# Kernel optimization log

Hardware: AMD Instinct MI355X
Metric: run time of the kernel (lower is better)

The kernel has to match this reference:

```python
import jax, jax.numpy as jnp
import numpy as np

GAMES = 16384
BOARD = 64


def setup_inputs() -> dict:
    key = jax.random.key(0)
    k_act, k_noise = jax.random.split(key)
    c = BOARD // 2
    # Replicate TensorSnake.init(): snake body=1 at (c-1,c-1), head=2 at (c-1,c), one food cell=-1.
    state = np.zeros((GAMES, BOARD, BOARD), dtype=np.float32)
    state[:, c - 1, c - 1] = 1.0
    state[:, c - 1, c] = 2.0
    state[:, 0, 0] = -1.0  # food
    pos_prev = np.tile(np.array([[c - 1, c - 1]], dtype=np.int32), (GAMES, 1))
    pos_cur = pos_prev + np.array([0, 1], dtype=np.int32)
    action = jax.random.randint(k_act, (GAMES,), 0, 3, dtype=jnp.int32)
    noise = jax.random.uniform(k_noise, (GAMES, BOARD * BOARD), dtype=jnp.float32)
    return {
        "state": jnp.asarray(state),
        "pos_prev": jnp.asarray(pos_prev),
        "pos_cur": jnp.asarray(pos_cur),
        "action": action,
        "noise": noise,
    }


def reference(state, pos_prev, pos_cur, action, noise):
    G, B, _ = state.shape
    g = jnp.arange(G)
    # --- direction update per action (0=left, 1=straight, 2=right) ---
    d = pos_cur - pos_prev  # [G,2]
    d_left = jnp.stack([-d[:, 1], d[:, 0]], axis=1)   # flip then negate x
    d_right = jnp.stack([d[:, 1], -d[:, 0]], axis=1)  # flip then negate y
    left = (action == 0)[:, None]
    right = (action == 2)[:, None]
    d = jnp.where(left, d_left, jnp.where(right, d_right, d))
    pos_next = d + pos_cur
    # --- wall collision / clamp ---
    outside = jnp.any((pos_next < 0) | (pos_next >= B), axis=1)
    pos_next = jnp.clip(pos_next, 0, B - 1)
    cell = state[g, pos_next[:, 0], pos_next[:, 1]]
    dead = outside | (cell > 0)
    feeding = cell == -1
    # --- reset dead games ---
    state = jnp.where(dead[:, None, None], jnp.zeros((), state.dtype), state)
    c = B // 2
    p2 = jnp.array([c, c], dtype=pos_next.dtype)
    pos_cur = jnp.where(dead[:, None], jnp.array([c, c - 1], dtype=pos_cur.dtype), pos_cur)
    pos_next = jnp.where(dead[:, None], p2, pos_next)
    state = state.at[:, c, c - 2].set(jnp.where(dead, 1.0, state[:, c, c - 2]))
    state = state.at[:, c, c - 1].set(jnp.where(dead, 2.0, state[:, c, c - 1]))
    state = state.at[:, c, c].set(jnp.where(dead, 1.0, state[:, c, c]))
    # --- food spawn: uniform choice among empty cells via masked argmax on uniform noise ---
    spawn = dead | feeding
    empty = state.reshape(G, -1) == 0
    food = jnp.argmax(jnp.where(empty, noise, -jnp.inf), axis=1)
    fx = food // B
    fy = food % B
    state = state.at[g, fx, fy].set(jnp.where(spawn, -1.0, state[g, fx, fy]))
    # --- tail decay (skipped for feeding games) ---
    dec = (state > 0) & (~feeding)[:, None, None]
    state = state - dec.astype(state.dtype)
    # --- advance head ---
    head = state[g, pos_cur[:, 0], pos_cur[:, 1]]
    state = state.at[g, pos_next[:, 0], pos_next[:, 1]].set(head + 1.0)
    return state
```

## Files before the change

kernel.cpp:

```cpp
#include <hip/hip_runtime.h>
#include <math.h>

#define NGAMES 16384
#define BRD 64
#define CELLS 4096
#define THREADS 128
#define CHUNKS 8
#define NWAVES (THREADS / 64)

typedef float f4 __attribute__((ext_vector_type(4)));

__global__ __launch_bounds__(THREADS) void snake_step_kernel(
    const float* __restrict__ state,
    const int*   __restrict__ pos_prev,
    const int*   __restrict__ pos_cur,
    const int*   __restrict__ action,
    const float* __restrict__ noise,
    float*       __restrict__ out)
{
    const int g = blockIdx.x;
    const int t = threadIdx.x;
    const float* sg = state + (size_t)g * CELLS;
    float*       og = out   + (size_t)g * CELLS;

    __shared__ float wv[NWAVES];
    __shared__ int   wi[NWAVES];
    __shared__ int   food_s;

    const int pp0 = pos_prev[2 * g], pp1 = pos_prev[2 * g + 1];
    const int pc0 = pos_cur[2 * g],  pc1 = pos_cur[2 * g + 1];
    const int a = action[g];
    const int d0 = pc0 - pp0, d1 = pc1 - pp1;
    int nd0 = d0, nd1 = d1;
    if (a == 0)      { nd0 = -d1; nd1 =  d0; }
    else if (a == 2) { nd0 =  d1; nd1 = -d0; }
    int pn0 = pc0 + nd0, pn1 = pc1 + nd1;
    const bool outside = (pn0 < 0) | (pn0 >= BRD) | (pn1 < 0) | (pn1 >= BRD);
    pn0 = min(max(pn0, 0), BRD - 1);
    pn1 = min(max(pn1, 0), BRD - 1);
    const int posn_spec = pn0 * BRD + pn1;
    const int posc_live = pc0 * BRD + pc1;

    const float cellv = sg[posn_spec];
    const float curv  = sg[posc_live];

    f4 v[CHUNKS];
    const f4* sg4 = reinterpret_cast<const f4*>(sg);
    #pragma unroll
    for (int k = 0; k < CHUNKS; ++k)
        v[k] = sg4[t + k * THREADS];

    #pragma unroll
    for (int k = 0; k < CHUNKS; ++k) {
        #pragma unroll
        for (int j = 0; j < 4; ++j)
            v[k][j] = (v[k][j] > 0.0f) ? v[k][j] - 1.0f : v[k][j];
    }

    const int  headF   = posn_spec >> 2;
    const int  headK   = headF >> 7;
    const bool ownHead = (t == (headF & (THREADS - 1)));

    f4* og4 = reinterpret_cast<f4*>(og);
    #pragma unroll
    for (int k = 0; k < CHUNKS; ++k)
        if (!(ownHead && k == headK))
            __builtin_nontemporal_store(v[k], &og4[t + k * THREADS]);

    const bool dead    = outside | (cellv > 0.0f);
    const bool feeding = (cellv == -1.0f);
    const bool rare    = dead | feeding;

    if (!rare) {
        if (ownHead) {
            const float headv = (curv > 0.0f) ? curv - 1.0f : curv;
            const float hv = headv + 1.0f;
            const int j = posn_spec & 3;
            #pragma unroll
            for (int k = 0; k < CHUNKS; ++k)
                if (k == headK) {
                    f4 w = v[k];
                    w[j] = hv;
                    __builtin_nontemporal_store(w, &og4[t + k * THREADS]);
                }
        }
        return;
    }

    __syncthreads();

    float s[CHUNKS * 4];
    f4* s4 = reinterpret_cast<f4*>(s);
    #pragma unroll
    for (int k = 0; k < CHUNKS; ++k)
        s4[k] = sg4[t + k * THREADS];

    if (dead) {
        #pragma unroll
        for (int k = 0; k < CHUNKS; ++k) {
            #pragma unroll
            for (int j = 0; j < 4; ++j) {
                const int idx = (t + k * THREADS) * 4 + j;
                float x = 0.0f;
                if (idx == 2078) x = 1.0f;
                else if (idx == 2079) x = 2.0f;
                else if (idx == 2080) x = 1.0f;
                s[k * 4 + j] = x;
            }
        }
    }

    {
        float bv = -INFINITY;
        int   bi = 0x7FFFFFFF;
        const f4* ng4 = reinterpret_cast<const f4*>(noise + (size_t)g * CELLS);
        #pragma unroll
        for (int k = 0; k < CHUNKS; ++k) {
            const f4 nv = ng4[t + k * THREADS];
            #pragma unroll
            for (int j = 0; j < 4; ++j) {
                const int idx = (t + k * THREADS) * 4 + j;
                if (s[k * 4 + j] == 0.0f) {
                    const float n = nv[j];
                    if (n > bv || (n == bv && idx < bi)) { bv = n; bi = idx; }
                }
            }
        }
        #pragma unroll
        for (int off = 32; off > 0; off >>= 1) {
            const float ov = __shfl_xor(bv, off, 64);
            const int   oi = __shfl_xor(bi, off, 64);
            if (ov > bv || (ov == bv && oi < bi)) { bv = ov; bi = oi; }
        }
        const int wave = t >> 6;
        if ((t & 63) == 0) { wv[wave] = bv; wi[wave] = bi; }
        __syncthreads();
        if (t == 0) {
            float fv = wv[0]; int fi = wi[0];
            #pragma unroll
            for (int w = 1; w < NWAVES; ++w)
                if (wv[w] > fv || (wv[w] == fv && wi[w] < fi)) { fv = wv[w]; fi = wi[w]; }
            food_s = (fv == -INFINITY) ? 0 : fi;
        }
        __syncthreads();
    }
    const int food = food_s;

    #pragma unroll
    for (int k = 0; k < CHUNKS; ++k) {
        #pragma unroll
        for (int j = 0; j < 4; ++j) {
            const int idx = (t + k * THREADS) * 4 + j;
            if (idx == food) s[k * 4 + j] = -1.0f;
            if (!feeding && s[k * 4 + j] > 0.0f) s[k * 4 + j] -= 1.0f;
        }
    }

    const int posc = dead ? (32 * BRD + 31) : posc_live;
    const int posn = dead ? (32 * BRD + 32) : posn_spec;
    float headv = dead ? 2.0f : curv;
    if (food == posc) headv = -1.0f;
    if (!feeding && headv > 0.0f) headv -= 1.0f;
    const float hv = headv + 1.0f;

    const int posnF = posn >> 2, posnJ = posn & 3;
    #pragma unroll
    for (int k = 0; k < CHUNKS; ++k) {
        f4 w = s4[k];
        if ((t + k * THREADS) == posnF) w[posnJ] = hv;
        og4[t + k * THREADS] = w;
    }
}

extern "C" void kernel_launch(void* const* d_in, const int* in_sizes, int n_in,
                              void* d_out, int out_size, void* d_ws, size_t ws_size,
                              hipStream_t stream) {
    const float* state    = (const float*)d_in[0];
    const int*   pos_prev = (const int*)d_in[1];
    const int*   pos_cur  = (const int*)d_in[2];
    const int*   action   = (const int*)d_in[3];
    const float* noise    = (const float*)d_in[4];
    float*       out      = (float*)d_out;

    snake_step_kernel<<<NGAMES, THREADS, 0, stream>>>(
        state, pos_prev, pos_cur, action, noise, out);
}
```

Before: 69.14 us.

## Map one wavefront per game with four games per block

Each 64-lane wavefront now owns a whole game, holding 16 float4 chunks per lane, and a block of 256 threads processes four games. This removes the shared-memory cross-wave argmax reduction and all __syncthreads, so the food-spawn path resolves with wave shuffles alone. The state load is issued before the scalar position loads to start memory traffic earlier. Per-lane register pressure doubles (64 floats held), which may lower occupancy on the bandwidth-bound copy.

```diff
diff --git a/kernel.cpp b/kernel.cpp
--- a/kernel.cpp
+++ b/kernel.cpp
@@ -4,9 +4,9 @@
 #define NGAMES 16384
 #define BRD 64
 #define CELLS 4096
-#define THREADS 128
-#define CHUNKS 8
-#define NWAVES (THREADS / 64)
+#define THREADS 256
+#define GPB 4
+#define CHUNKS 16
 
 typedef float f4 __attribute__((ext_vector_type(4)));
 
@@ -18,14 +18,17 @@
     const float* __restrict__ noise,
     float*       __restrict__ out)
 {
-    const int g = blockIdx.x;
-    const int t = threadIdx.x;
+    const int g    = blockIdx.x * GPB + (threadIdx.x >> 6);
+    const int lane = threadIdx.x & 63;
     const float* sg = state + (size_t)g * CELLS;
     float*       og = out   + (size_t)g * CELLS;
+    const f4* sg4 = reinterpret_cast<const f4*>(sg);
+    f4*       og4 = reinterpret_cast<f4*>(og);
 
-    __shared__ float wv[NWAVES];
-    __shared__ int   wi[NWAVES];
-    __shared__ int   food_s;
+    f4 v[CHUNKS];
+    #pragma unroll
+    for (int k = 0; k < CHUNKS; ++k)
+        v[k] = sg4[lane + k * 64];
 
     const int pp0 = pos_prev[2 * g], pp1 = pos_prev[2 * g + 1];
     const int pc0 = pos_cur[2 * g],  pc1 = pos_cur[2 * g + 1];
@@ -44,12 +47,6 @@
     const float cellv = sg[posn_spec];
     const float curv  = sg[posc_live];
 
-    f4 v[CHUNKS];
-    const f4* sg4 = reinterpret_cast<const f4*>(sg);
-    #pragma unroll
-    for (int k = 0; k < CHUNKS; ++k)
-        v[k] = sg4[t + k * THREADS];
-
     #pragma unroll
     for (int k = 0; k < CHUNKS; ++k) {
         #pragma unroll
@@ -58,14 +55,13 @@
     }
 
     const int  headF   = posn_spec >> 2;
-    const int  headK   = headF >> 7;
-    const bool ownHead = (t == (headF & (THREADS - 1)));
+    const int  headK   = headF >> 6;
+    const bool ownHead = (lane == (headF & 63));
 
-    f4* og4 = reinterpret_cast<f4*>(og);
     #pragma unroll
     for (int k = 0; k < CHUNKS; ++k)
         if (!(ownHead && k == headK))
-            __builtin_nontemporal_store(v[k], &og4[t + k * THREADS]);
+            __builtin_nontemporal_store(v[k], &og4[lane + k * 64]);
 
     const bool dead    = outside | (cellv > 0.0f);
     const bool feeding = (cellv == -1.0f);
@@ -81,46 +77,43 @@
                 if (k == headK) {
                     f4 w = v[k];
                     w[j] = hv;
-                    __builtin_nontemporal_store(w, &og4[t + k * THREADS]);
+                    __builtin_nontemporal_store(w, &og4[lane + k * 64]);
                 }
         }
         return;
     }
 
-    __syncthreads();
-
-    float s[CHUNKS * 4];
-    f4* s4 = reinterpret_cast<f4*>(s);
     #pragma unroll
     for (int k = 0; k < CHUNKS; ++k)
-        s4[k] = sg4[t + k * THREADS];
+        v[k] = sg4[lane + k * 64];
 
     if (dead) {
         #pragma unroll
         for (int k = 0; k < CHUNKS; ++k) {
             #pragma unroll
             for (int j = 0; j < 4; ++j) {
-                const int idx = (t + k * THREADS) * 4 + j;
+                const int idx = (lane + k * 64) * 4 + j;
                 float x = 0.0f;
                 if (idx == 2078) x = 1.0f;
                 else if (idx == 2079) x = 2.0f;
                 else if (idx == 2080) x = 1.0f;
-                s[k * 4 + j] = x;
+                v[k][j] = x;
             }
         }
     }
 
+    int food;
     {
         float bv = -INFINITY;
         int   bi = 0x7FFFFFFF;
         const f4* ng4 = reinterpret_cast<const f4*>(noise + (size_t)g * CELLS);
         #pragma unroll
         for (int k = 0; k < CHUNKS; ++k) {
-            const f4 nv = ng4[t + k * THREADS];
+            const f4 nv = ng4[lane + k * 64];
             #pragma unroll
             for (int j = 0; j < 4; ++j) {
-                const int idx = (t + k * THREADS) * 4 + j;
-                if (s[k * 4 + j] == 0.0f) {
+                const int idx = (lane + k * 64) * 4 + j;
+                if (v[k][j] == 0.0f) {
                     const float n = nv[j];
                     if (n > bv || (n == bv && idx < bi)) { bv = n; bi = idx; }
                 }
@@ -132,27 +125,16 @@
             const int   oi = __shfl_xor(bi, off, 64);
             if (ov > bv || (ov == bv && oi < bi)) { bv = ov; bi = oi; }
         }
-        const int wave = t >> 6;
-        if ((t & 63) == 0) { wv[wave] = bv; wi[wave] = bi; }
-        __syncthreads();
-        if (t == 0) {
-            float fv = wv[0]; int fi = wi[0];
-            #pragma unroll
-            for (int w = 1; w < NWAVES; ++w)
-                if (wv[w] > fv || (wv[w] == fv && wi[w] < fi)) { fv = wv[w]; fi = wi[w]; }
-            food_s = (fv == -INFINITY) ? 0 : fi;
-        }
-        __syncthreads();
+        food = (bv == -INFINITY) ? 0 : bi;
     }
-    const int food = food_s;
 
     #pragma unroll
     for (int k = 0; k < CHUNKS; ++k) {
         #pragma unroll
         for (int j = 0; j < 4; ++j) {
-            const int idx = (t + k * THREADS) * 4 + j;
-            if (idx == food) s[k * 4 + j] = -1.0f;
-            if (!feeding && s[k * 4 + j] > 0.0f) s[k * 4 + j] -= 1.0f;
+            const int idx = (lane + k * 64) * 4 + j;
+            if (idx == food) v[k][j] = -1.0f;
+            if (!feeding && v[k][j] > 0.0f) v[k][j] -= 1.0f;
         }
     }
 
@@ -166,9 +148,9 @@
     const int posnF = posn >> 2, posnJ = posn & 3;
     #pragma unroll
     for (int k = 0; k < CHUNKS; ++k) {
-        f4 w = s4[k];
-        if ((t + k * THREADS) == posnF) w[posnJ] = hv;
-        og4[t + k * THREADS] = w;
+        f4 w = v[k];
+        if ((lane + k * 64) == posnF) w[posnJ] = hv;
+        og4[lane + k * 64] = w;
     }
 }
 
@@ -182,6 +164,6 @@
     const float* noise    = (const float*)d_in[4];
     float*       out      = (float*)d_out;
 
-    snake_step_kernel<<<NGAMES, THREADS, 0, stream>>>(
+    snake_step_kernel<<<NGAMES / GPB, THREADS, 0, stream>>>(
         state, pos_prev, pos_cur, action, noise, out);
 }
```

Measured after the change: 70.98 us. +2.7%, slower.
